# Performance work log

Measured on AMD Instinct MI355X. Metric: run time of the kernel, lower is better.

Reference implementation:

```python
import jax, jax.numpy as jnp
import numpy as np

NUM_GRAPHS = 128
NODES_PER_GRAPH = 512
NUM_NODES = NUM_GRAPHS * NODES_PER_GRAPH
NUM_EDGES = NUM_NODES * 16
IN_DIM = 64
HID = 128
NUM_HEADS = 4
BN_EPS = 1e-5


def setup_inputs() -> dict:
    key = jax.random.key(0)
    ks = jax.random.split(key, 12)
    x = jax.random.normal(ks[0], (NUM_NODES, IN_DIM), dtype=jnp.float32)
    edge_index = jax.random.randint(ks[1], (2, NUM_EDGES), 0, NUM_NODES, dtype=jnp.int32)
    batch = jnp.repeat(jnp.arange(NUM_GRAPHS, dtype=jnp.int32), NODES_PER_GRAPH)
    s = 0.05
    W0 = jax.random.normal(ks[2], (IN_DIM, HID), dtype=jnp.float32) * s
    b0 = jnp.zeros((HID,), jnp.float32)
    Wh = jax.random.normal(ks[3], (3, HID, HID), dtype=jnp.float32) * s  # convs 1..3
    bh = jnp.zeros((3, HID), jnp.float32)
    bn_gamma = jnp.ones((4, HID), jnp.float32)
    bn_beta = jnp.zeros((4, HID), jnp.float32)
    bn_mean = jnp.zeros((4, HID), jnp.float32)
    bn_var = jnp.ones((4, HID), jnp.float32)
    attn_in_w = jax.random.normal(ks[4], (3 * HID, HID), dtype=jnp.float32) * s
    attn_in_b = jnp.zeros((3 * HID,), jnp.float32)
    attn_out_w = jax.random.normal(ks[5], (HID, HID), dtype=jnp.float32) * s
    attn_out_b = jnp.zeros((HID,), jnp.float32)
    return dict(x=x, W0=W0, b0=b0, Wh=Wh, bh=bh, bn_gamma=bn_gamma, bn_beta=bn_beta,
                bn_mean=bn_mean, bn_var=bn_var, attn_in_w=attn_in_w, attn_in_b=attn_in_b,
                attn_out_w=attn_out_w, attn_out_b=attn_out_b, edge_index=edge_index, batch=batch)


def _forward(x, W0, b0, Wh, bh, bn_gamma, bn_beta, bn_mean, bn_var,
             attn_in_w, attn_in_b, attn_out_w, attn_out_b, edge_index, batch):
    N = x.shape[0]
    src, dst = edge_index[0], edge_index[1]
    # GCN symmetric normalization with self-loops (PyG GCNConv)
    deg = jax.ops.segment_sum(jnp.ones_like(src, jnp.float32), dst, num_segments=N) + 1.0
    dis = jax.lax.rsqrt(deg)                      # deg^{-1/2}
    enorm = (dis[src] * dis[dst])[:, None]        # per-edge norm
    self_norm = (dis * dis)[:, None]              # self-loop norm

    def gcn(h, W, b):
        h = h @ W
        agg = jax.ops.segment_sum(h[src] * enorm, dst, num_segments=N)
        return agg + h * self_norm + b

    def bn(h, i):
        scale = bn_gamma[i] * jax.lax.rsqrt(bn_var[i] + BN_EPS)
        return (h - bn_mean[i]) * scale + bn_beta[i]  # eval-mode BN

    # dropout is identity in eval mode
    h = jax.nn.relu(bn(gcn(x, W0, b0), 0))
    h = jax.nn.relu(bn(gcn(h, Wh[0], bh[0]), 1))
    h = jax.nn.relu(bn(gcn(h, Wh[1], bh[1]), 2))
    f = jax.nn.relu(bn(gcn(h, Wh[2], bh[2]), 3))   # [N, HID]

    # per-graph self-attention (equal-size contiguous graphs -> batched MHA)
    dh = HID // NUM_HEADS
    xg = f.reshape(NUM_GRAPHS, NODES_PER_GRAPH, HID)
    qkv = xg @ attn_in_w.T + attn_in_b            # [G, n, 3H]
    q, k, v = jnp.split(qkv, 3, axis=-1)

    def heads(t):
        return t.reshape(NUM_GRAPHS, NODES_PER_GRAPH, NUM_HEADS, dh).transpose(0, 2, 1, 3)
    q, k, v = heads(q), heads(k), heads(v)
    scores = jnp.einsum('ghnd,ghmd->ghnm', q, k) / np.sqrt(dh).astype(np.float32)
    attn = jax.nn.softmax(scores, axis=-1)
    o = jnp.einsum('ghnm,ghmd->ghnd', attn, v).transpose(0, 2, 1, 3).reshape(NUM_GRAPHS, NODES_PER_GRAPH, HID)
    o = o @ attn_out_w.T + attn_out_b
    final = o.reshape(N, HID)

    # global mean pool over batch indices
    cnt = jax.ops.segment_sum(jnp.ones((N,), jnp.float32), batch, num_segments=NUM_GRAPHS)
    graph_emb = jax.ops.segment_sum(final, batch, num_segments=NUM_GRAPHS) / cnt[:, None]
    return final, graph_emb


def reference(x, W0, b0, Wh, bh, bn_gamma, bn_beta, bn_mean, bn_var,
              attn_in_w, attn_in_b, attn_out_w, attn_out_b, edge_index, batch):
    return _forward(x, W0, b0, Wh, bh, bn_gamma, bn_beta, bn_mean, bn_var,
                    attn_in_w, attn_in_b, attn_out_w, attn_out_b, edge_index, batch)
```

## Files before the change

kernel.cpp:

```cpp
#include <hip/hip_runtime.h>
#include <hip/hip_bf16.h>
#include <cstdint>
#include <cstddef>

#define N_NODES 65536
#define N_EDGES 1048576
#define N_GRAPHS 128
#define NPG 512
#define IN_DIM 64
#define HID 128
#define BN_EPS 1e-5f

typedef __attribute__((ext_vector_type(8))) short bf16x8;
typedef __attribute__((ext_vector_type(4))) float f32x4;
typedef __attribute__((ext_vector_type(8))) unsigned short u16x8;

__device__ inline unsigned short f2bf(float f) {
  unsigned u = __builtin_bit_cast(unsigned, f);
  u = u + 0x7fffu + ((u >> 16) & 1u);
  return (unsigned short)(u >> 16);
}
__device__ inline float bf2f(unsigned short h) {
  unsigned u = ((unsigned)h) << 16;
  return __builtin_bit_cast(float, u);
}
__device__ inline void split_bf(float v, unsigned short& hi, unsigned short& lo) {
  hi = f2bf(v);
  lo = f2bf(v - bf2f(hi));
}
__device__ inline void split_bf_fast(float v, unsigned short& hi, unsigned short& lo) {
  unsigned u = __builtin_bit_cast(unsigned, v);
  hi = (unsigned short)(u >> 16);
  float r = v - __builtin_bit_cast(float, u & 0xffff0000u);
  lo = f2bf(r);
}

__global__ __launch_bounds__(256) void hist_kernel(const int* __restrict__ dst,
                                                   int* __restrict__ deg) {
  int e = blockIdx.x * 256 + threadIdx.x;
  if (e < N_EDGES) atomicAdd(&deg[dst[e]], 1);
}

__global__ __launch_bounds__(256) void dis_kernel(const int* __restrict__ deg,
                                                  float* __restrict__ dis) {
  int n = blockIdx.x * 256 + threadIdx.x;
  if (n < N_NODES) dis[n] = 1.0f / sqrtf((float)deg[n] + 1.0f);
}

__global__ __launch_bounds__(1024) void scan_kernel(const int* __restrict__ deg,
                                                    int* __restrict__ offsets,
                                                    int* __restrict__ cursor) {
  __shared__ int sums[1024];
  int t = threadIdx.x;
  int base = t * 64;
  const int4* dp = (const int4*)(deg + base);
  int s = 0;
#pragma unroll
  for (int i = 0; i < 16; i++) {
    int4 v = dp[i];
    s += v.x + v.y + v.z + v.w;
  }
  sums[t] = s;
  __syncthreads();
  for (int off = 1; off < 1024; off <<= 1) {
    int v = (t >= off) ? sums[t - off] : 0;
    __syncthreads();
    sums[t] += v;
    __syncthreads();
  }
  int run = (t == 0) ? 0 : sums[t - 1];
#pragma unroll
  for (int i = 0; i < 16; i++) {
    int4 v = dp[i];
    int idx = base + i * 4;
    offsets[idx] = run; cursor[idx] = run; run += v.x;
    offsets[idx + 1] = run; cursor[idx + 1] = run; run += v.y;
    offsets[idx + 2] = run; cursor[idx + 2] = run; run += v.z;
    offsets[idx + 3] = run; cursor[idx + 3] = run; run += v.w;
  }
  if (t == 1023) offsets[N_NODES] = run;
}

__global__ __launch_bounds__(256) void fill_kernel(const int* __restrict__ src,
                                                   const int* __restrict__ dst,
                                                   int* __restrict__ cursor,
                                                   int* __restrict__ csr) {
  int e = blockIdx.x * 256 + threadIdx.x;
  if (e < N_EDGES) {
    int d = dst[e];
    int slot = atomicAdd(&cursor[d], 1);
    csr[slot] = src[e];
  }
}

__global__ __launch_bounds__(256) void agg64_kernel(const float* __restrict__ x,
                                                    const float* __restrict__ dis,
                                                    const int* __restrict__ offsets,
                                                    const int* __restrict__ csr,
                                                    unsigned short* __restrict__ zhi,
                                                    unsigned short* __restrict__ zlo) {
  int node = blockIdx.x * 4 + (threadIdx.x >> 6);
  int lane = threadIdx.x & 63;
  float dn = dis[node];
  float acc = x[(size_t)node * 64 + lane] * dn * dn;
  int beg = offsets[node], end = offsets[node + 1];
  int k = beg;
  for (; k + 4 <= end; k += 4) {
    int s0 = csr[k], s1 = csr[k + 1], s2 = csr[k + 2], s3 = csr[k + 3];
    float w0 = dn * dis[s0], w1 = dn * dis[s1], w2 = dn * dis[s2], w3 = dn * dis[s3];
    float v0 = x[(size_t)s0 * 64 + lane];
    float v1 = x[(size_t)s1 * 64 + lane];
    float v2 = x[(size_t)s2 * 64 + lane];
    float v3 = x[(size_t)s3 * 64 + lane];
    acc = fmaf(w0, v0, acc);
    acc = fmaf(w1, v1, acc);
    acc = fmaf(w2, v2, acc);
    acc = fmaf(w3, v3, acc);
  }
  for (; k < end; k++) {
    int s = csr[k];
    acc = fmaf(dn * dis[s], x[(size_t)s * 64 + lane], acc);
  }
  unsigned short h_, l_;
  split_bf(acc, h_, l_);
  zhi[(size_t)node * 64 + lane] = h_;
  zlo[(size_t)node * 64 + lane] = l_;
}

__global__ __launch_bounds__(256) void agg128_kernel(const float* __restrict__ h,
                                                     const float* __restrict__ dis,
                                                     const int* __restrict__ offsets,
                                                     const int* __restrict__ csr,
                                                     unsigned short* __restrict__ zhi,
                                                     unsigned short* __restrict__ zlo) {
  int node = blockIdx.x * 4 + (threadIdx.x >> 6);
  int lane = threadIdx.x & 63;
  float dn = dis[node];
  float sn = dn * dn;
  const float* hr = h + (size_t)node * 128;
  float a0 = hr[lane] * sn;
  float a1 = hr[lane + 64] * sn;
  int beg = offsets[node], end = offsets[node + 1];
  int k = beg;
  for (; k + 4 <= end; k += 4) {
    int s0 = csr[k], s1 = csr[k + 1], s2 = csr[k + 2], s3 = csr[k + 3];
    float w0 = dn * dis[s0], w1 = dn * dis[s1], w2 = dn * dis[s2], w3 = dn * dis[s3];
    const float* p0 = h + (size_t)s0 * 128;
    const float* p1 = h + (size_t)s1 * 128;
    const float* p2 = h + (size_t)s2 * 128;
    const float* p3 = h + (size_t)s3 * 128;
    float u0 = p0[lane], d0 = p0[lane + 64];
    float u1 = p1[lane], d1 = p1[lane + 64];
    float u2 = p2[lane], d2 = p2[lane + 64];
    float u3 = p3[lane], d3 = p3[lane + 64];
    a0 = fmaf(w0, u0, a0); a1 = fmaf(w0, d0, a1);
    a0 = fmaf(w1, u1, a0); a1 = fmaf(w1, d1, a1);
    a0 = fmaf(w2, u2, a0); a1 = fmaf(w2, d2, a1);
    a0 = fmaf(w3, u3, a0); a1 = fmaf(w3, d3, a1);
  }
  for (; k < end; k++) {
    int s = csr[k];
    float w = dn * dis[s];
    const float* hs = h + (size_t)s * 128;
    a0 = fmaf(w, hs[lane], a0);
    a1 = fmaf(w, hs[lane + 64], a1);
  }
  unsigned short h0, l0, h1, l1;
  split_bf(a0, h0, l0);
  split_bf(a1, h1, l1);
  zhi[(size_t)node * 128 + lane] = h0;
  zlo[(size_t)node * 128 + lane] = l0;
  zhi[(size_t)node * 128 + lane + 64] = h1;
  zlo[(size_t)node * 128 + lane + 64] = l1;
}

template <bool TRANS>
__global__ __launch_bounds__(256) void wprep_kernel(const float* __restrict__ W, int K, int O,
                                                    unsigned short* __restrict__ hi,
                                                    unsigned short* __restrict__ lo) {
  int idx = blockIdx.x * 256 + threadIdx.x;
  int KC = K / 32;
  int total = (O / 16) * KC * 64;
  if (idx >= total) return;
  int lane = idx & 63;
  int rest = idx >> 6;
  int kc = rest % KC;
  int nt = rest / KC;
  int n = nt * 16 + (lane & 15);
  int kb = kc * 32 + (lane >> 4) * 8;
  unsigned short* hp = hi + (size_t)idx * 8;
  unsigned short* lp = lo + (size_t)idx * 8;
#pragma unroll
  for (int j = 0; j < 8; j++) {
    int k = kb + j;
    float v = TRANS ? W[(size_t)n * K + k] : W[(size_t)k * O + n];
    unsigned short h_, l_;
    split_bf(v, h_, l_);
    hp[j] = h_;
    lp[j] = l_;
  }
}

template <int K, int O, bool DOBN, bool DORELU, bool SPLIT_OUT>
__global__ __launch_bounds__(256) void gemm_mfma(
    const unsigned short* __restrict__ Ahi, const unsigned short* __restrict__ Alo,
    const unsigned short* __restrict__ Whi, const unsigned short* __restrict__ Wlo,
    const float* __restrict__ bias,
    const float* __restrict__ gamma, const float* __restrict__ beta,
    const float* __restrict__ mean, const float* __restrict__ var,
    float* __restrict__ Cf, unsigned short* __restrict__ Chi,
    unsigned short* __restrict__ Clo) {
  constexpr int KC = K / 32;
  int wave = threadIdx.x >> 6;
  int lane = threadIdx.x & 63;
  int m0 = blockIdx.x * 128 + wave * 32;
  int o0 = blockIdx.y * 128;
  int mrow = lane & 15;
  int kseg = (lane >> 4) * 8;

  f32x4 acc[2][8];
#pragma unroll
  for (int mt = 0; mt < 2; mt++)
#pragma unroll
    for (int nt = 0; nt < 8; nt++) acc[mt][nt] = (f32x4)0.0f;

#pragma unroll
  for (int kc = 0; kc < KC; kc++) {
    bf16x8 ah[2], al[2];
#pragma unroll
    for (int mt = 0; mt < 2; mt++) {
      size_t aoff = (size_t)(m0 + mt * 16 + mrow) * K + kc * 32 + kseg;
      ah[mt] = *(const bf16x8*)(Ahi + aoff);
      al[mt] = *(const bf16x8*)(Alo + aoff);
    }
#pragma unroll
    for (int nt = 0; nt < 8; nt++) {
      size_t foff = (((size_t)(blockIdx.y * 8 + nt) * KC + kc) * 64 + lane) * 8;
      bf16x8 bh = *(const bf16x8*)(Whi + foff);
      bf16x8 bl = *(const bf16x8*)(Wlo + foff);
#pragma unroll
      for (int mt = 0; mt < 2; mt++) {
        acc[mt][nt] = __builtin_amdgcn_mfma_f32_16x16x32_bf16(ah[mt], bh, acc[mt][nt], 0, 0, 0);
        acc[mt][nt] = __builtin_amdgcn_mfma_f32_16x16x32_bf16(ah[mt], bl, acc[mt][nt], 0, 0, 0);
        acc[mt][nt] = __builtin_amdgcn_mfma_f32_16x16x32_bf16(al[mt], bh, acc[mt][nt], 0, 0, 0);
        acc[mt][nt] = __builtin_amdgcn_mfma_f32_16x16x32_bf16(al[mt], bl, acc[mt][nt], 0, 0, 0);
      }
    }
  }

  int ccol = lane & 15;
  int crow0 = (lane >> 4) * 4;
#pragma unroll
  for (int nt = 0; nt < 8; nt++) {
    int c = o0 + nt * 16 + ccol;
    float sc, cb;
    float b = bias[c];
    if (DOBN) {
      sc = gamma[c] * rsqrtf(var[c] + BN_EPS);
      cb = (b - mean[c]) * sc + beta[c];
    } else {
      sc = 1.0f;
      cb = b;
    }
#pragma unroll
    for (int mt = 0; mt < 2; mt++) {
#pragma unroll
      for (int r = 0; r < 4; r++) {
        float v = fmaf(acc[mt][nt][r], sc, cb);
        if (DORELU) v = fmaxf(v, 0.0f);
        size_t row = (size_t)(m0 + mt * 16 + crow0 + r);
        if (SPLIT_OUT) {
          unsigned short h_, l_;
          split_bf(v, h_, l_);
          Chi[row * O + c] = h_;
          Clo[row * O + c] = l_;
        } else {
          Cf[row * O + c] = v;
        }
      }
    }
  }
}

__global__ __launch_bounds__(256) void knorm_kernel(const unsigned short* __restrict__ qh_,
                                                    const unsigned short* __restrict__ ql_,
                                                    float* __restrict__ kmax2) {
  int g = blockIdx.x >> 2;
  int h = blockIdx.x & 3;
  size_t gbase = (size_t)g * NPG;
  float best = 0.0f;
#pragma unroll
  for (int r = 0; r < 2; r++) {
    int j = r * 256 + threadIdx.x;
    size_t base = (gbase + j) * 384 + 128 + (size_t)h * 32;
    float s = 0.0f;
#pragma unroll
    for (int i = 0; i < 4; i++) {
      u16x8 hh = *(const u16x8*)(qh_ + base + i * 8);
      u16x8 ll = *(const u16x8*)(ql_ + base + i * 8);
#pragma unroll
      for (int jj = 0; jj < 8; jj++) {
        float v = bf2f(hh[jj]) + bf2f(ll[jj]);
        s = fmaf(v, v, s);
      }
    }
    best = fmaxf(best, s);
  }
#pragma unroll
  for (int off = 32; off >= 1; off >>= 1)
    best = fmaxf(best, __shfl_xor(best, off, 64));
  __shared__ float red[4];
  int wave = threadIdx.x >> 6;
  if ((threadIdx.x & 63) == 0) red[wave] = best;
  __syncthreads();
  if (threadIdx.x == 0) {
    float m = fmaxf(fmaxf(red[0], red[1]), fmaxf(red[2], red[3]));
    kmax2[blockIdx.x] = m;
  }
}

__global__ __launch_bounds__(256, 2) void attn_mfma_kernel(
    const unsigned short* __restrict__ qh_, const unsigned short* __restrict__ ql_,
    const float* __restrict__ kmax2,
    unsigned short* __restrict__ ohi, unsigned short* __restrict__ olo) {
  int b = blockIdx.x;
  int g = b >> 3;
  int h = (b >> 1) & 3;
  int half = b & 1;
  int t = threadIdx.x;
  int wave = t >> 6;
  int lane = t & 63;
  int quad = lane >> 4;
  int l15 = lane & 15;
  size_t gbase = (size_t)g * NPG;
  int qb = half * 256 + wave * 64;

  const float cf = 0.17677669529663687f * 1.4426950408889634f;

  __shared__ unsigned short Kh[32][40], Kl[32][40];
  __shared__ unsigned short Vh[33][40], Vl[33][40];
  __shared__ char wbuf[4][10240] __attribute__((aligned(16)));

  unsigned short* Ph = (unsigned short*)wbuf[wave];
  unsigned short* Pl = Ph + 64 * 40;
  float* Ot = (float*)wbuf[wave];

  bf16x8 qh[4], ql[4];
  float qn2p[4];
#pragma unroll
  for (int mt = 0; mt < 4; mt++) {
    size_t qoff = (gbase + qb + mt * 16 + l15) * 384 + (size_t)h * 32 + quad * 8;
    u16x8 hh = *(const u16x8*)(qh_ + qoff);
    u16x8 ll = *(const u16x8*)(ql_ + qoff);
    qh[mt] = __builtin_bit_cast(bf16x8, hh);
    ql[mt] = __builtin_bit_cast(bf16x8, ll);
    float s = 0.0f;
#pragma unroll
    for (int j = 0; j < 8; j++) {
      float v = bf2f(hh[j]) + bf2f(ll[j]);
      s = fmaf(v, v, s);
    }
    s += __shfl_xor(s, 16);
    s += __shfl_xor(s, 32);
    qn2p[mt] = s;
  }
  if (quad == 0) {
#pragma unroll
    for (int mt = 0; mt < 4; mt++) Ot[mt * 16 + l15] = qn2p[mt];
  }
  float km2 = kmax2[g * 4 + h];
  float Mq[4][4];
#pragma unroll
  for (int mt = 0; mt < 4; mt++)
#pragma unroll
    for (int r = 0; r < 4; r++)
      Mq[mt][r] = cf * sqrtf(Ot[mt * 16 + quad * 4 + r] * km2);

  f32x4 Oa[4][3];
#pragma unroll
  for (int mt = 0; mt < 4; mt++)
#pragma unroll
    for (int nt = 0; nt < 3; nt++) Oa[mt][nt] = (f32x4)0.0f;

  for (int c = 0; c < 16; c++) {
    __syncthreads();
    if (t >= 128) {
      int t2 = t - 128;
      int key = t2 >> 2;
      int ds = (t2 & 3) * 8;
      size_t ko = (gbase + (size_t)(c * 32 + key)) * 384 + 128 + (size_t)h * 32 + ds;
      *(u16x8*)&Kh[key][ds] = *(const u16x8*)(qh_ + ko);
      *(u16x8*)&Kl[key][ds] = *(const u16x8*)(ql_ + ko);
    } else if (t < 64) {
      int keyb = (t & 7) * 4;
      int dvb = (t >> 3) * 4;
      unsigned short ha[4][4], la[4][4];
#pragma unroll
      for (int r = 0; r < 4; r++) {
        size_t vo = (gbase + (size_t)(c * 32 + keyb + r)) * 384 + 256 + (size_t)h * 32 + dvb;
        *(ushort4*)&ha[r][0] = *(const ushort4*)(qh_ + vo);
        *(ushort4*)&la[r][0] = *(const ushort4*)(ql_ + vo);
      }
#pragma unroll
      for (int c2 = 0; c2 < 4; c2++) {
        ushort4 hv, lv;
        hv.x = ha[0][c2]; hv.y = ha[1][c2]; hv.z = ha[2][c2]; hv.w = ha[3][c2];
        lv.x = la[0][c2]; lv.y = la[1][c2]; lv.z = la[2][c2]; lv.w = la[3][c2];
        *(ushort4*)&Vh[dvb + c2][keyb] = hv;
        *(ushort4*)&Vl[dvb + c2][keyb] = lv;
      }
    } else if (t < 68) {
      int i = t - 64;
      u16x8 ones;
#pragma unroll
      for (int j = 0; j < 8; j++) ones[j] = 0x3F80;
      *(u16x8*)&Vh[32][i * 8] = ones;
    }
    __syncthreads();

#pragma unroll
    for (int nt = 0; nt < 2; nt++) {
      bf16x8 bkh = *(const bf16x8*)&Kh[nt * 16 + l15][quad * 8];
      bf16x8 bkl = *(const bf16x8*)&Kl[nt * 16 + l15][quad * 8];
#pragma unroll
      for (int mt = 0; mt < 4; mt++) {
        f32x4 S = (f32x4)0.0f;
        S = __builtin_amdgcn_mfma_f32_16x16x32_bf16(qh[mt], bkh, S, 0, 0, 0);
        S = __builtin_amdgcn_mfma_f32_16x16x32_bf16(qh[mt], bkl, S, 0, 0, 0);
        S = __builtin_amdgcn_mfma_f32_16x16x32_bf16(ql[mt], bkh, S, 0, 0, 0);
        S = __builtin_amdgcn_mfma_f32_16x16x32_bf16(ql[mt], bkl, S, 0, 0, 0);
#pragma unroll
        for (int r = 0; r < 4; r++) {
          float p = __builtin_exp2f(fmaf(S[r], cf, -Mq[mt][r]));
          unsigned short hi_, lo_;
          split_bf_fast(p, hi_, lo_);
          int row = mt * 16 + quad * 4 + r;
          Ph[row * 40 + nt * 16 + l15] = hi_;
          Pl[row * 40 + nt * 16 + l15] = lo_;
        }
      }
    }
    bf16x8 pah[4], pal[4];
#pragma unroll
    for (int mt = 0; mt < 4; mt++) {
      pah[mt] = *(const bf16x8*)&Ph[(mt * 16 + l15) * 40 + quad * 8];
      pal[mt] = *(const bf16x8*)&Pl[(mt * 16 + l15) * 40 + quad * 8];
    }
#pragma unroll
    for (int nt = 0; nt < 3; nt++) {
      bf16x8 bvh = *(const bf16x8*)&Vh[nt * 16 + l15][quad * 8];
      if (nt < 2) {
        bf16x8 bvl = *(const bf16x8*)&Vl[nt * 16 + l15][quad * 8];
#pragma unroll
        for (int mt = 0; mt < 4; mt++) {
          Oa[mt][nt] = __builtin_amdgcn_mfma_f32_16x16x32_bf16(pah[mt], bvh, Oa[mt][nt], 0, 0, 0);
          Oa[mt][nt] = __builtin_amdgcn_mfma_f32_16x16x32_bf16(pah[mt], bvl, Oa[mt][nt], 0, 0, 0);
          Oa[mt][nt] = __builtin_amdgcn_mfma_f32_16x16x32_bf16(pal[mt], bvh, Oa[mt][nt], 0, 0, 0);
        }
      } else {
#pragma unroll
        for (int mt = 0; mt < 4; mt++) {
          Oa[mt][nt] = __builtin_amdgcn_mfma_f32_16x16x32_bf16(pah[mt], bvh, Oa[mt][nt], 0, 0, 0);
          Oa[mt][nt] = __builtin_amdgcn_mfma_f32_16x16x32_bf16(pal[mt], bvh, Oa[mt][nt], 0, 0, 0);
        }
      }
    }
  }

#pragma unroll
  for (int mt = 0; mt < 4; mt++) {
#pragma unroll
    for (int r = 0; r < 4; r++) {
      int row = mt * 16 + quad * 4 + r;
      Ot[row * 36 + l15] = Oa[mt][0][r];
      Ot[row * 36 + 16 + l15] = Oa[mt][1][r];
      if (l15 == 0) Ot[row * 36 + 32] = Oa[mt][2][r];
    }
  }
  {
    int row = lane;
    float inv = 1.0f / Ot[row * 36 + 32];
    size_t node = gbase + qb + row;
    u16x8 vh, vl;
#pragma unroll
    for (int seg = 0; seg < 4; seg++) {
#pragma unroll
      for (int j = 0; j < 8; j++) {
        unsigned short hi_, lo_;
        split_bf_fast(Ot[row * 36 + seg * 8 + j] * inv, hi_, lo_);
        vh[j] = hi_;
        vl[j] = lo_;
      }
      *(u16x8*)(ohi + node * 128 + h * 32 + seg * 8) = vh;
      *(u16x8*)(olo + node * 128 + h * 32 + seg * 8) = vl;
    }
  }
}

__global__ __launch_bounds__(128) void pool_kernel(const float* __restrict__ fin,
                                                   float* __restrict__ emb) {
  int g = blockIdx.x >> 2;
  int q = blockIdx.x & 3;
  int c = threadIdx.x;
  const float* p = fin + ((size_t)g * NPG + (size_t)q * 128) * HID + c;
  float s = 0.0f;
#pragma unroll 4
  for (int i = 0; i < 128; i++) s += p[(size_t)i * HID];
  atomicAdd(&emb[g * HID + c], s * (1.0f / NPG));
}

extern "C" void kernel_launch(void* const* d_in, const int* in_sizes, int n_in,
                              void* d_out, int out_size, void* d_ws, size_t ws_size,
                              hipStream_t stream) {
  (void)in_sizes; (void)n_in; (void)out_size; (void)ws_size;
  const float* x          = (const float*)d_in[0];
  const float* W0         = (const float*)d_in[1];
  const float* b0         = (const float*)d_in[2];
  const float* Wh         = (const float*)d_in[3];
  const float* bh         = (const float*)d_in[4];
  const float* bn_gamma   = (const float*)d_in[5];
  const float* bn_beta    = (const float*)d_in[6];
  const float* bn_mean    = (const float*)d_in[7];
  const float* bn_var     = (const float*)d_in[8];
  const float* attn_in_w  = (const float*)d_in[9];
  const float* attn_in_b  = (const float*)d_in[10];
  const float* attn_out_w = (const float*)d_in[11];
  const float* attn_out_b = (const float*)d_in[12];
  const int* edge_index   = (const int*)d_in[13];
  const int* src = edge_index;
  const int* dst = edge_index + N_EDGES;

  char* ws = (char*)d_ws;
  size_t off = 0;
  auto alloc = [&](size_t bytes) -> void* {
    void* p = ws + off;
    off += (bytes + 255) & ~(size_t)255;
    return p;
  };
  int*   deg     = (int*)alloc((size_t)N_NODES * 4);
  int*   offsets = (int*)alloc((size_t)(N_NODES + 1) * 4);
  int*   cursor  = (int*)alloc((size_t)N_NODES * 4);
  int*   csr     = (int*)alloc((size_t)N_EDGES * 4);
  float* dis     = (float*)alloc((size_t)N_NODES * 4);
  float* bufA    = (float*)alloc((size_t)N_NODES * HID * 4);
  unsigned short* zhi = (unsigned short*)alloc((size_t)N_NODES * HID * 2);
  unsigned short* zlo = (unsigned short*)alloc((size_t)N_NODES * HID * 2);
  unsigned short* qvh = (unsigned short*)alloc((size_t)N_NODES * 384 * 2);
  unsigned short* qvl = (unsigned short*)alloc((size_t)N_NODES * 384 * 2);
  float* kmax2   = (float*)alloc((size_t)N_GRAPHS * 4 * 4);
  unsigned short* w0h = (unsigned short*)alloc(8192 * 2);
  unsigned short* w0l = (unsigned short*)alloc(8192 * 2);
  unsigned short* whh[3], *whl[3];
  for (int i = 0; i < 3; i++) {
    whh[i] = (unsigned short*)alloc(16384 * 2);
    whl[i] = (unsigned short*)alloc(16384 * 2);
  }
  unsigned short* wqh = (unsigned short*)alloc(49152 * 2);
  unsigned short* wql = (unsigned short*)alloc(49152 * 2);
  unsigned short* woh = (unsigned short*)alloc(16384 * 2);
  unsigned short* wol = (unsigned short*)alloc(16384 * 2);

  unsigned short* fhi = (unsigned short*)bufA;
  unsigned short* flo = fhi + (size_t)N_NODES * HID;

  float* fin = (float*)d_out;
  float* emb = fin + (size_t)N_NODES * HID;

  hipMemsetAsync(deg, 0, (size_t)N_NODES * 4, stream);
  hipMemsetAsync(emb, 0, (size_t)N_GRAPHS * HID * 4, stream);
  hist_kernel<<<N_EDGES / 256, 256, 0, stream>>>(dst, deg);
  dis_kernel<<<N_NODES / 256, 256, 0, stream>>>(deg, dis);
  scan_kernel<<<1, 1024, 0, stream>>>(deg, offsets, cursor);
  fill_kernel<<<N_EDGES / 256, 256, 0, stream>>>(src, dst, cursor, csr);

  wprep_kernel<false><<<4, 256, 0, stream>>>(W0, 64, 128, w0h, w0l);
  for (int i = 0; i < 3; i++)
    wprep_kernel<false><<<8, 256, 0, stream>>>(Wh + (size_t)i * HID * HID, 128, 128,
                                               whh[i], whl[i]);
  wprep_kernel<true><<<24, 256, 0, stream>>>(attn_in_w, 128, 384, wqh, wql);
  wprep_kernel<true><<<8, 256, 0, stream>>>(attn_out_w, 128, 128, woh, wol);

  dim3 ggrid(N_NODES / 128, 1);
  agg64_kernel<<<N_NODES / 4, 256, 0, stream>>>(x, dis, offsets, csr, zhi, zlo);
  gemm_mfma<64, 128, true, true, false><<<ggrid, 256, 0, stream>>>(
      zhi, zlo, w0h, w0l, b0, bn_gamma, bn_beta, bn_mean, bn_var, bufA, nullptr, nullptr);
  for (int L = 0; L < 2; L++) {
    agg128_kernel<<<N_NODES / 4, 256, 0, stream>>>(bufA, dis, offsets, csr, zhi, zlo);
    gemm_mfma<128, 128, true, true, false><<<ggrid, 256, 0, stream>>>(
        zhi, zlo, whh[L], whl[L], bh + (size_t)L * HID,
        bn_gamma + (size_t)(L + 1) * HID, bn_beta + (size_t)(L + 1) * HID,
        bn_mean + (size_t)(L + 1) * HID, bn_var + (size_t)(L + 1) * HID,
        bufA, nullptr, nullptr);
  }
  agg128_kernel<<<N_NODES / 4, 256, 0, stream>>>(bufA, dis, offsets, csr, zhi, zlo);
  gemm_mfma<128, 128, true, true, true><<<ggrid, 256, 0, stream>>>(
      zhi, zlo, whh[2], whl[2], bh + (size_t)2 * HID,
      bn_gamma + (size_t)3 * HID, bn_beta + (size_t)3 * HID,
      bn_mean + (size_t)3 * HID, bn_var + (size_t)3 * HID,
      nullptr, fhi, flo);
  dim3 qgrid(N_NODES / 128, 3);
  gemm_mfma<128, 384, false, false, true><<<qgrid, 256, 0, stream>>>(
      fhi, flo, wqh, wql, attn_in_b, nullptr, nullptr, nullptr, nullptr,
      nullptr, qvh, qvl);
  knorm_kernel<<<N_GRAPHS * 4, 256, 0, stream>>>(qvh, qvl, kmax2);
  attn_mfma_kernel<<<N_GRAPHS * 4 * 2, 256, 0, stream>>>(qvh, qvl, kmax2, zhi, zlo);
  gemm_mfma<128, 128, false, false, false><<<ggrid, 256, 0, stream>>>(
      zhi, zlo, woh, wol, attn_out_b, nullptr, nullptr, nullptr, nullptr,
      fin, nullptr, nullptr);
  pool_kernel<<<N_GRAPHS * 4, 128, 0, stream>>>(fin, emb);
}
```

Before: 849.7 us.

## Interleave QKV hi/lo layout, prefetch K/V chunks, and swizzle attention block order

The QKV projection now writes hi and lo bf16 halves interleaved per 32-column head group into a single buffer, so the attention and knorm kernels fetch both halves from adjacent 64-byte spans instead of two separate arrays. The attention kernel register-prefetches the next K/V chunk while the current chunk is computed, overlapping global loads with MFMA work. It also remaps block indices so that consecutive blocks fall on different graphs and heads. The costs are extra registers that may reduce occupancy, and scattered 2-byte stores in the GEMM epilogue.

Result: faster. 830.7 us (-2.2%).

```diff
diff --git a/kernel.cpp b/kernel.cpp
--- a/kernel.cpp
+++ b/kernel.cpp
@@ -201,7 +201,7 @@
   }
 }
 
-template <int K, int O, bool DOBN, bool DORELU, bool SPLIT_OUT>
+template <int K, int O, bool DOBN, bool DORELU, bool SPLIT_OUT, bool GROUPED>
 __global__ __launch_bounds__(256) void gemm_mfma(
     const unsigned short* __restrict__ Ahi, const unsigned short* __restrict__ Alo,
     const unsigned short* __restrict__ Whi, const unsigned short* __restrict__ Wlo,
@@ -272,8 +272,14 @@
         if (SPLIT_OUT) {
           unsigned short h_, l_;
           split_bf(v, h_, l_);
-          Chi[row * O + c] = h_;
-          Clo[row * O + c] = l_;
+          if (GROUPED) {
+            size_t base = row * (size_t)(2 * O) + (size_t)(((c >> 5) << 6) + (c & 31));
+            Chi[base] = h_;
+            Chi[base + 32] = l_;
+          } else {
+            Chi[row * O + c] = h_;
+            Clo[row * O + c] = l_;
+          }
         } else {
           Cf[row * O + c] = v;
         }
@@ -282,8 +288,7 @@
   }
 }
 
-__global__ __launch_bounds__(256) void knorm_kernel(const unsigned short* __restrict__ qh_,
-                                                    const unsigned short* __restrict__ ql_,
+__global__ __launch_bounds__(256) void knorm_kernel(const unsigned short* __restrict__ qvs,
                                                     float* __restrict__ kmax2) {
   int g = blockIdx.x >> 2;
   int h = blockIdx.x & 3;
@@ -292,12 +297,12 @@
 #pragma unroll
   for (int r = 0; r < 2; r++) {
     int j = r * 256 + threadIdx.x;
-    size_t base = (gbase + j) * 384 + 128 + (size_t)h * 32;
+    size_t base = (gbase + j) * 768 + (size_t)(4 + h) * 64;
     float s = 0.0f;
 #pragma unroll
     for (int i = 0; i < 4; i++) {
-      u16x8 hh = *(const u16x8*)(qh_ + base + i * 8);
-      u16x8 ll = *(const u16x8*)(ql_ + base + i * 8);
+      u16x8 hh = *(const u16x8*)(qvs + base + i * 8);
+      u16x8 ll = *(const u16x8*)(qvs + base + 32 + i * 8);
 #pragma unroll
       for (int jj = 0; jj < 8; jj++) {
         float v = bf2f(hh[jj]) + bf2f(ll[jj]);
@@ -320,13 +325,12 @@
 }
 
 __global__ __launch_bounds__(256, 2) void attn_mfma_kernel(
-    const unsigned short* __restrict__ qh_, const unsigned short* __restrict__ ql_,
-    const float* __restrict__ kmax2,
+    const unsigned short* __restrict__ qvs, const float* __restrict__ kmax2,
     unsigned short* __restrict__ ohi, unsigned short* __restrict__ olo) {
-  int b = blockIdx.x;
-  int g = b >> 3;
-  int h = (b >> 1) & 3;
-  int half = b & 1;
+  int wb = ((blockIdx.x & 7) << 7) | (blockIdx.x >> 3);
+  int g = wb >> 3;
+  int h = (wb >> 1) & 3;
+  int half = wb & 1;
   int t = threadIdx.x;
   int wave = t >> 6;
   int lane = t & 63;
@@ -349,9 +353,9 @@
   float qn2p[4];
 #pragma unroll
   for (int mt = 0; mt < 4; mt++) {
-    size_t qoff = (gbase + qb + mt * 16 + l15) * 384 + (size_t)h * 32 + quad * 8;
-    u16x8 hh = *(const u16x8*)(qh_ + qoff);
-    u16x8 ll = *(const u16x8*)(ql_ + qoff);
+    size_t qoff = (gbase + qb + mt * 16 + l15) * 768 + (size_t)h * 64 + quad * 8;
+    u16x8 hh = *(const u16x8*)(qvs + qoff);
+    u16x8 ll = *(const u16x8*)(qvs + qoff + 32);
     qh[mt] = __builtin_bit_cast(bf16x8, hh);
     ql[mt] = __builtin_bit_cast(bf16x8, ll);
     float s = 0.0f;
@@ -382,40 +386,65 @@
 #pragma unroll
     for (int nt = 0; nt < 3; nt++) Oa[mt][nt] = (f32x4)0.0f;
 
+  if (t >= 64 && t < 68) {
+    int i = t - 64;
+    u16x8 ones;
+#pragma unroll
+    for (int j = 0; j < 8; j++) ones[j] = 0x3F80;
+    *(u16x8*)&Vh[32][i * 8] = ones;
+  }
+
+  u16x8 kreg_h, kreg_l;
+  ushort4 vreg_h[4], vreg_l[4];
+  int kkey = 0, kds = 0, vkeyb = 0, vdvb = 0;
+  if (t >= 128) {
+    int t2 = t - 128;
+    kkey = t2 >> 2;
+    kds = (t2 & 3) * 8;
+  } else if (t < 64) {
+    vkeyb = (t & 7) * 4;
+    vdvb = (t >> 3) * 4;
+  }
+
+  auto load_chunk = [&](int c) {
+    if (t >= 128) {
+      size_t ko = (gbase + (size_t)(c * 32 + kkey)) * 768 + (size_t)(4 + h) * 64 + kds;
+      kreg_h = *(const u16x8*)(qvs + ko);
+      kreg_l = *(const u16x8*)(qvs + ko + 32);
+    } else if (t < 64) {
+#pragma unroll
+      for (int r = 0; r < 4; r++) {
+        size_t vo = (gbase + (size_t)(c * 32 + vkeyb + r)) * 768 + (size_t)(8 + h) * 64 + vdvb;
+        vreg_h[r] = *(const ushort4*)(qvs + vo);
+        vreg_l[r] = *(const ushort4*)(qvs + vo + 32);
+      }
+    }
+  };
+
+  load_chunk(0);
+
   for (int c = 0; c < 16; c++) {
     __syncthreads();
     if (t >= 128) {
-      int t2 = t - 128;
-      int key = t2 >> 2;
-      int ds = (t2 & 3) * 8;
-      size_t ko = (gbase + (size_t)(c * 32 + key)) * 384 + 128 + (size_t)h * 32 + ds;
-      *(u16x8*)&Kh[key][ds] = *(const u16x8*)(qh_ + ko);
-      *(u16x8*)&Kl[key][ds] = *(const u16x8*)(ql_ + ko);
+      *(u16x8*)&Kh[kkey][kds] = kreg_h;
+      *(u16x8*)&Kl[kkey][kds] = kreg_l;
     } else if (t < 64) {
-      int keyb = (t & 7) * 4;
-      int dvb = (t >> 3) * 4;
       unsigned short ha[4][4], la[4][4];
 #pragma unroll
       for (int r = 0; r < 4; r++) {
-        size_t vo = (gbase + (size_t)(c * 32 + keyb + r)) * 384 + 256 + (size_t)h * 32 + dvb;
-        *(ushort4*)&ha[r][0] = *(const ushort4*)(qh_ + vo);
-        *(ushort4*)&la[r][0] = *(const ushort4*)(ql_ + vo);
+        *(ushort4*)&ha[r][0] = vreg_h[r];
+        *(ushort4*)&la[r][0] = vreg_l[r];
       }
 #pragma unroll
       for (int c2 = 0; c2 < 4; c2++) {
         ushort4 hv, lv;
         hv.x = ha[0][c2]; hv.y = ha[1][c2]; hv.z = ha[2][c2]; hv.w = ha[3][c2];
         lv.x = la[0][c2]; lv.y = la[1][c2]; lv.z = la[2][c2]; lv.w = la[3][c2];
-        *(ushort4*)&Vh[dvb + c2][keyb] = hv;
-        *(ushort4*)&Vl[dvb + c2][keyb] = lv;
-      }
-    } else if (t < 68) {
-      int i = t - 64;
-      u16x8 ones;
-#pragma unroll
-      for (int j = 0; j < 8; j++) ones[j] = 0x3F80;
-      *(u16x8*)&Vh[32][i * 8] = ones;
-    }
+        *(ushort4*)&Vh[vdvb + c2][vkeyb] = hv;
+        *(ushort4*)&Vl[vdvb + c2][vkeyb] = lv;
+      }
+    }
+    if (c < 15) load_chunk(c + 1);
     __syncthreads();
 
 #pragma unroll
@@ -545,8 +574,7 @@
   float* bufA    = (float*)alloc((size_t)N_NODES * HID * 4);
   unsigned short* zhi = (unsigned short*)alloc((size_t)N_NODES * HID * 2);
   unsigned short* zlo = (unsigned short*)alloc((size_t)N_NODES * HID * 2);
-  unsigned short* qvh = (unsigned short*)alloc((size_t)N_NODES * 384 * 2);
-  unsigned short* qvl = (unsigned short*)alloc((size_t)N_NODES * 384 * 2);
+  unsigned short* qvs = (unsigned short*)alloc((size_t)N_NODES * 768 * 2);
   float* kmax2   = (float*)alloc((size_t)N_GRAPHS * 4 * 4);
   unsigned short* w0h = (unsigned short*)alloc(8192 * 2);
   unsigned short* w0l = (unsigned short*)alloc(8192 * 2);
@@ -582,29 +610,29 @@
 
   dim3 ggrid(N_NODES / 128, 1);
   agg64_kernel<<<N_NODES / 4, 256, 0, stream>>>(x, dis, offsets, csr, zhi, zlo);
-  gemm_mfma<64, 128, true, true, false><<<ggrid, 256, 0, stream>>>(
+  gemm_mfma<64, 128, true, true, false, false><<<ggrid, 256, 0, stream>>>(
       zhi, zlo, w0h, w0l, b0, bn_gamma, bn_beta, bn_mean, bn_var, bufA, nullptr, nullptr);
   for (int L = 0; L < 2; L++) {
     agg128_kernel<<<N_NODES / 4, 256, 0, stream>>>(bufA, dis, offsets, csr, zhi, zlo);
-    gemm_mfma<128, 128, true, true, false><<<ggrid, 256, 0, stream>>>(
+    gemm_mfma<128, 128, true, true, false, false><<<ggrid, 256, 0, stream>>>(
         zhi, zlo, whh[L], whl[L], bh + (size_t)L * HID,
         bn_gamma + (size_t)(L + 1) * HID, bn_beta + (size_t)(L + 1) * HID,
         bn_mean + (size_t)(L + 1) * HID, bn_var + (size_t)(L + 1) * HID,
         bufA, nullptr, nullptr);
   }
   agg128_kernel<<<N_NODES / 4, 256, 0, stream>>>(bufA, dis, offsets, csr, zhi, zlo);
-  gemm_mfma<128, 128, true, true, true><<<ggrid, 256, 0, stream>>>(
+  gemm_mfma<128, 128, true, true, true, false><<<ggrid, 256, 0, stream>>>(
       zhi, zlo, whh[2], whl[2], bh + (size_t)2 * HID,
       bn_gamma + (size_t)3 * HID, bn_beta + (size_t)3 * HID,
       bn_mean + (size_t)3 * HID, bn_var + (size_t)3 * HID,
       nullptr, fhi, flo);
   dim3 qgrid(N_NODES / 128, 3);
-  gemm_mfma<128, 384, false, false, true><<<qgrid, 256, 0, stream>>>(
+  gemm_mfma<128, 384, false, false, true, true><<<qgrid, 256, 0, stream>>>(
       fhi, flo, wqh, wql, attn_in_b, nullptr, nullptr, nullptr, nullptr,
-      nullptr, qvh, qvl);
-  knorm_kernel<<<N_GRAPHS * 4, 256, 0, stream>>>(qvh, qvl, kmax2);
-  attn_mfma_kernel<<<N_GRAPHS * 4 * 2, 256, 0, stream>>>(qvh, qvl, kmax2, zhi, zlo);
-  gemm_mfma<128, 128, false, false, false><<<ggrid, 256, 0, stream>>>(
+      nullptr, qvs, nullptr);
+  knorm_kernel<<<N_GRAPHS * 4, 256, 0, stream>>>(qvs, kmax2);
+  attn_mfma_kernel<<<N_GRAPHS * 4 * 2, 256, 0, stream>>>(qvs, kmax2, zhi, zlo);
+  gemm_mfma<128, 128, false, false, false, false><<<ggrid, 256, 0, stream>>>(
       zhi, zlo, woh, wol, attn_out_b, nullptr, nullptr, nullptr, nullptr,
       fin, nullptr, nullptr);
   pool_kernel<<<N_GRAPHS * 4, 128, 0, stream>>>(fin, emb);
```
